# Kernel optimization log

Measured on AMD Instinct MI355X. Metric: run time of the kernel, lower is better.

Reference implementation:

```python
import jax, jax.numpy as jnp
import numpy as np

N_HEADS = 16
D_K = 64
DIM = 1024
NEG = -1e12
LN_EPS = 1e-5


def setup_inputs() -> dict:
    key = jax.random.key(0)
    ks = jax.random.split(key, 8)
    B, S, D = 2, 2048, DIM
    H, K = N_HEADS, D_K
    f = lambda k, shp: jax.random.normal(k, shp, dtype=jnp.float32)
    scale = 0.02
    return {
        "input_Q": f(ks[0], (B, S, D)),
        "input_K": f(ks[1], (B, S, D)),
        "input_V": f(ks[2], (B, S, D)),
        "attention_mask": jax.random.randint(ks[3], (B, S), 0, 2, dtype=jnp.int32),
        "W_Q": f(ks[4], (H * K, D)) * scale,  # nn.Linear weight layout [out, in]
        "W_K": f(ks[5], (H * K, D)) * scale,
        "W_V": f(ks[6], (H * K, D)) * scale,
        "W_O": f(ks[7], (D, H * K)) * scale,
        "gamma": jnp.ones((D,), jnp.float32),
        "beta": jnp.zeros((D,), jnp.float32),
    }


def reference(input_Q, input_K, input_V, attention_mask, W_Q, W_K, W_V, W_O, gamma, beta):
    B, S, D = input_Q.shape

    def proj(x, W):  # [B,S,D] @ [HK,D]^T -> [B,H,S,K]
        return (x @ W.T).reshape(B, S, N_HEADS, D_K).transpose(0, 2, 1, 3)

    Q = proj(input_Q, W_Q)
    K = proj(input_K, W_K)
    V = proj(input_V, W_V)

    scores = jnp.einsum('bhqk,bhsk->bhqs', Q, K) / np.float32(np.sqrt(D_K))

    # Faithful reproduction of scores_mask (including its inverted-looking logic):
    # mask = clamp(padding_mask + strict_upper_tri - 1, min=0); scores += (1-mask)*NEG
    am = attention_mask.astype(scores.dtype)[:, None, None, :]          # [B,1,1,S]
    low_tri = jnp.triu(jnp.ones((S, S), scores.dtype), k=1)             # 1 - tril(ones)
    m = jnp.maximum(am + low_tri - 1.0, 0.0)
    scores = scores + (1.0 - m) * NEG

    attn = jax.nn.softmax(scores, axis=-1)
    ctx = jnp.einsum('bhqs,bhsk->bhqk', attn, V)                        # [B,H,S,K]
    ctx = ctx.transpose(0, 2, 1, 3).reshape(B, S, N_HEADS * D_K)

    out = ctx @ W_O.T + input_Q                                         # fc + residual
    mu = jnp.mean(out, axis=-1, keepdims=True)
    var = jnp.var(out, axis=-1, keepdims=True)
    return (out - mu) / jnp.sqrt(var + LN_EPS) * gamma + beta
```

## Files before the change

### kernel.cpp

```cpp
#include <hip/hip_runtime.h>

#define NH    16
#define DK    64
#define DIM   1024
#define BATCH 2
#define SEQ   2048
#define MROWS (BATCH*SEQ)
#define QSCALE 0.18033688011112043f
#define SENT   -44.0f
#define PCONST 5.684341886080802e-14f

typedef unsigned short bfraw;
typedef __attribute__((ext_vector_type(8))) __bf16 bf16x8;
typedef __attribute__((ext_vector_type(4))) __bf16 bf16x4;
typedef __attribute__((ext_vector_type(8))) unsigned short u16x8;
typedef __attribute__((ext_vector_type(4))) unsigned short u16x4;
typedef __attribute__((ext_vector_type(4))) short s16x4;
typedef __attribute__((ext_vector_type(4))) float f32x4;

__device__ __forceinline__ float bf2f(bfraw u) {
    union { unsigned int i; float f; } x; x.i = ((unsigned int)u) << 16; return x.f;
}
__device__ __forceinline__ bfraw f2bf(float f) {
    union { float f; unsigned int i; } x; x.f = f;
    unsigned int r = x.i + 0x7FFFu + ((x.i >> 16) & 1u);
    return (bfraw)(r >> 16);
}
__device__ __forceinline__ bfraw f2bf_trunc(float f) {
    union { float f; unsigned int i; } x; x.f = f;
    return (bfraw)(x.i >> 16);
}
__device__ __forceinline__ float fexp2(float x) {
#if __has_builtin(__builtin_amdgcn_exp2f)
    return __builtin_amdgcn_exp2f(x);
#else
    return exp2f(x);
#endif
}

__device__ __forceinline__ f32x4 mfma16(s16x4 a, s16x4 b, f32x4 c) {
#if __has_builtin(__builtin_amdgcn_mfma_f32_16x16x16_bf16)
    union { s16x4 s; bf16x4 h; } ua, ub; ua.s = a; ub.s = b;
    return __builtin_amdgcn_mfma_f32_16x16x16_bf16(ua.h, ub.h, c, 0, 0, 0);
#elif __has_builtin(__builtin_amdgcn_mfma_f32_16x16x16bf16_1k)
    return __builtin_amdgcn_mfma_f32_16x16x16bf16_1k(a, b, c, 0, 0, 0);
#else
    asm("v_mfma_f32_16x16x16_bf16 %0, %1, %2, %0" : "+v"(c) : "v"(a), "v"(b));
    return c;
#endif
}

__device__ __forceinline__ float block_reduce(float val, float* rbuf, int op) {
    const int lane = threadIdx.x & 63, wave = threadIdx.x >> 6;
    #pragma unroll
    for (int off = 32; off; off >>= 1) {
        float o = __shfl_xor(val, off, 64);
        val = op ? (val + o) : fmaxf(val, o);
    }
    if (lane == 0) rbuf[wave] = val;
    __syncthreads();
    float r = op ? (rbuf[0] + rbuf[1] + rbuf[2] + rbuf[3])
                 : fmaxf(fmaxf(rbuf[0], rbuf[1]), fmaxf(rbuf[2], rbuf[3]));
    __syncthreads();
    return r;
}

__global__ __launch_bounds__(256) void cvt_kernel(
        const float* __restrict__ x0, const float* __restrict__ x1, const float* __restrict__ x2,
        const float* __restrict__ w0, const float* __restrict__ w1, const float* __restrict__ w2,
        const float* __restrict__ w3, bfraw* __restrict__ Xb, bfraw* __restrict__ Wb) {
    const int t = blockIdx.y;
    const float* src; bfraw* dst; int n;
    if (t < 3) { src = (t == 0) ? x0 : (t == 1) ? x1 : x2; dst = Xb + t * (MROWS * DIM); n = MROWS * DIM; }
    else { int u = t - 3; src = (u == 0) ? w0 : (u == 1) ? w1 : (u == 2) ? w2 : w3;
           dst = Wb + u * (DIM * DIM); n = DIM * DIM; }
    int idx = (blockIdx.x * 256 + threadIdx.x) * 8;
    if (idx >= n) return;
    f32x4 a = *(const f32x4*)(src + idx);
    f32x4 b = *(const f32x4*)(src + idx + 4);
    u16x8 o;
    #pragma unroll
    for (int j = 0; j < 4; j++) { o[j] = f2bf(a[j]); o[4 + j] = f2bf(b[j]); }
    *(u16x8*)(dst + idx) = o;
}

__device__ __forceinline__ void gemm128(const bfraw* __restrict__ A, const bfraw* __restrict__ B,
                                        int m0, int n0, f32x4 acc[4][4]) {
    __shared__ __align__(16) bfraw As[2][128 * 64];
    __shared__ __align__(16) bfraw Bs[2][128 * 64];
    const int tid = threadIdx.x, wave = tid >> 6;
    const int lane = tid & 63, lrow = lane & 15, quad = lane >> 4;
    const int wy = wave >> 1, wx = wave & 1;
    const int swz = lrow & 7;
    const int srow = tid >> 2;
    const int cg0  = (tid & 3) << 1;
    const int gc   = cg0 << 3;
    const int e7   = srow & 7;
    const int o0 = ((cg0 ^ e7) << 3), o1 = (((cg0 | 1) ^ e7) << 3);

    const bfraw* pa0 = A + (m0 + srow) * DIM + gc;
    const bfraw* pa1 = A + (m0 + 64 + srow) * DIM + gc;
    const bfraw* pb0 = B + (n0 + srow) * DIM + gc;
    const bfraw* pb1 = B + (n0 + 64 + srow) * DIM + gc;

    #pragma unroll
    for (int i = 0; i < 4; i++)
        #pragma unroll
        for (int j = 0; j < 4; j++) { f32x4 z = {0.f, 0.f, 0.f, 0.f}; acc[i][j] = z; }

    u16x8 ha0[4], hb0[4], ha1[4], hb1[4];

    auto LOAD = [&](u16x8 ha[4], u16x8 hb[4], int kk) {
        ha[0] = *(const u16x8*)(pa0 + kk);     ha[1] = *(const u16x8*)(pa0 + kk + 8);
        ha[2] = *(const u16x8*)(pa1 + kk);     ha[3] = *(const u16x8*)(pa1 + kk + 8);
        hb[0] = *(const u16x8*)(pb0 + kk);     hb[1] = *(const u16x8*)(pb0 + kk + 8);
        hb[2] = *(const u16x8*)(pb1 + kk);     hb[3] = *(const u16x8*)(pb1 + kk + 8);
    };
    auto STORE = [&](bfraw* Ad, bfraw* Bd, u16x8 ha[4], u16x8 hb[4]) {
        *(u16x8*)&Ad[srow * 64 + o0]        = ha[0];
        *(u16x8*)&Ad[srow * 64 + o1]        = ha[1];
        *(u16x8*)&Ad[(64 + srow) * 64 + o0] = ha[2];
        *(u16x8*)&Ad[(64 + srow) * 64 + o1] = ha[3];
        *(u16x8*)&Bd[srow * 64 + o0]        = hb[0];
        *(u16x8*)&Bd[srow * 64 + o1]        = hb[1];
        *(u16x8*)&Bd[(64 + srow) * 64 + o0] = hb[2];
        *(u16x8*)&Bd[(64 + srow) * 64 + o1] = hb[3];
    };
    auto COMPUTE = [&](const bfraw* Ad, const bfraw* Bd) {
        #pragma unroll
        for (int ks = 0; ks < 2; ks++) {
            const int c = (ks << 2) | quad;
            bf16x8 af[4], bfg[4];
            #pragma unroll
            for (int mi = 0; mi < 4; mi++)
                af[mi] = *(const bf16x8*)&Ad[(wy * 64 + mi * 16 + lrow) * 64 + ((c ^ swz) << 3)];
            #pragma unroll
            for (int ni = 0; ni < 4; ni++)
                bfg[ni] = *(const bf16x8*)&Bd[(wx * 64 + ni * 16 + lrow) * 64 + ((c ^ swz) << 3)];
            #pragma unroll
            for (int mi = 0; mi < 4; mi++)
                #pragma unroll
                for (int ni = 0; ni < 4; ni++)
                    acc[mi][ni] = __builtin_amdgcn_mfma_f32_16x16x32_bf16(af[mi], bfg[ni], acc[mi][ni], 0, 0, 0);
        }
    };

    LOAD(ha0, hb0, 0);
    LOAD(ha1, hb1, 64);

    #pragma unroll
    for (int m2 = 0; m2 < DIM / 128; m2++) {
        const int k0 = m2 * 128;
        STORE(As[0], Bs[0], ha0, hb0);
        if (k0 + 128 < DIM) LOAD(ha0, hb0, k0 + 128);
        __syncthreads();
        COMPUTE(As[0], Bs[0]);
        STORE(As[1], Bs[1], ha1, hb1);
        if (k0 + 192 < DIM) LOAD(ha1, hb1, k0 + 192);
        __syncthreads();
        COMPUTE(As[1], Bs[1]);
    }
}

__global__ __launch_bounds__(256) void qkv_gemm(
        const bfraw* __restrict__ Xb, const bfraw* __restrict__ Wb,
        bfraw* __restrict__ Qp, bfraw* __restrict__ Kp, bfraw* __restrict__ Vt) {
    const int which = blockIdx.z;
    const bfraw* A = Xb + which * (MROWS * DIM);
    const bfraw* B = Wb + which * (DIM * DIM);
    bfraw* O = (which == 0) ? Qp : (which == 1) ? Kp : Vt;
    const int m0 = blockIdx.x * 128, n0 = blockIdx.y * 128;
    f32x4 acc[4][4];
    gemm128(A, B, m0, n0, acc);
    const int lane = threadIdx.x & 63, wave = threadIdx.x >> 6;
    const int lrow = lane & 15, quad = lane >> 4;
    const int wy = wave >> 1, wx = wave & 1;
    const float scale = (which == 0) ? QSCALE : 1.0f;
    #pragma unroll
    for (int mi = 0; mi < 4; mi++)
        #pragma unroll
        for (int ni = 0; ni < 4; ni++)
            #pragma unroll
            for (int i = 0; i < 4; i++) {
                int m = m0 + wy * 64 + mi * 16 + quad * 4 + i;
                int n = n0 + wx * 64 + ni * 16 + lrow;
                int b = m >> 11, s = m & (SEQ - 1), h = n >> 6, kk = n & (DK - 1);
                bfraw v = f2bf(acc[mi][ni][i] * scale);
                if (which == 2) O[(((b * NH + h) * DK) + kk) * SEQ + s] = v;
                else            O[(((b * NH + h) * SEQ) + s) * DK + kk] = v;
            }
}

__global__ __launch_bounds__(256) void vsum_kernel(const bfraw* __restrict__ Vt,
                                                   float* __restrict__ Scum) {
    __shared__ float Ts[32][65];
    const int bh = blockIdx.x, tid = threadIdx.x;
    const int d = tid & 63, part = tid >> 6;
    const bfraw* vrow = Vt + (bh * DK + d) * SEQ;
    for (int qt = part * 8; qt < part * 8 + 8; qt++) {
        float s = 0.f;
        #pragma unroll
        for (int j = 0; j < 64; j += 8) {
            u16x8 v = *(const u16x8*)(vrow + qt * 64 + j);
            #pragma unroll
            for (int e = 0; e < 8; e++) s += bf2f(v[e]);
        }
        Ts[qt][d] = s;
    }
    __syncthreads();
    if (tid < 64) {
        float run = 0.f;
        for (int qt = 0; qt < 32; qt++) {
            Scum[(bh * 32 + qt) * 64 + tid] = run;
            run += Ts[qt][tid];
        }
    }
}

__global__ __launch_bounds__(256) void attn_flash(
        const bfraw* __restrict__ Qp, const bfraw* __restrict__ Kp, const bfraw* __restrict__ Vt,
        const float* __restrict__ Scum, const int* __restrict__ mask, bfraw* __restrict__ Ctx) {
    __shared__ __align__(16) bfraw Ks[2][64 * 64];
    __shared__ __align__(16) bfraw Vs[2][64 * 64];
    __shared__ unsigned short Mk[SEQ];
    const int bh = blockIdx.x, yy = blockIdx.y;
    const int gg = yy >> 3, jj = yy & 7;
    const int qt = (gg == 0) ? jj : (gg == 1) ? (31 - jj) : (gg == 2) ? (8 + jj) : (23 - jj);
    const int b = bh >> 4, h = bh & 15;
    const int tid = threadIdx.x, wave = tid >> 6, lane = tid & 63;
    const int lrow = lane & 15, quad = lane >> 4;
    const int baseK = ((b * NH + h) * SEQ) * DK;
    const int baseV = ((b * NH + h) * DK) * SEQ;
    const int qbase = qt * 64 + wave * 16;
    const int q_ln  = qbase + lrow;
    const int diagKt = qt * 64;
    const int ldr = tid >> 2;
    const int cg0 = (tid & 3) << 1;
    const int ldc = cg0 << 3;
    const int e7 = ldr & 7;
    const int cl0 = ((cg0 ^ e7) << 3), cl1 = (((cg0 | 1) ^ e7) << 3);

    for (int i = tid; i < SEQ; i += 256) Mk[i] = (unsigned short)(mask[b * SEQ + i] != 0);

    bf16x8 qf[2];
    qf[0] = *(const bf16x8*)(Qp + baseK + (qbase + lrow) * DK + quad * 8);
    qf[1] = *(const bf16x8*)(Qp + baseK + (qbase + lrow) * DK + 32 + quad * 8);

    f32x4 Oa[4];
    #pragma unroll
    for (int nd = 0; nd < 4; nd++) {
        f32x4 sv = *(const f32x4*)&Scum[(bh * 32 + qt) * 64 + nd * 16 + quad * 4];
        #pragma unroll
        for (int i = 0; i < 4; i++) Oa[nd][i] = PCONST * sv[i];
    }
    float lsum = 0.f;

    const int nt = (SEQ - diagKt) >> 6;
    int kt0 = diagKt;
    u16x8 k0 = *(const u16x8*)(Kp + baseK + (kt0 + ldr) * DK + ldc);
    u16x8 k1 = *(const u16x8*)(Kp + baseK + (kt0 + ldr) * DK + ldc + 8);
    u16x8 v0 = *(const u16x8*)(Vt + baseV + ldr * SEQ + kt0 + ldc);
    u16x8 v1 = *(const u16x8*)(Vt + baseV + ldr * SEQ + kt0 + ldc + 8);

    for (int t = 0; t < nt; t++, kt0 += 64) {
        bfraw* Kb = Ks[t & 1];
        bfraw* Vb = Vs[t & 1];
        *(u16x8*)&Kb[ldr * 64 + cl0] = k0;
        *(u16x8*)&Kb[ldr * 64 + cl1] = k1;
        *(u16x8*)&Vb[ldr * 64 + cl0] = v0;
        *(u16x8*)&Vb[ldr * 64 + cl1] = v1;
        if (t + 1 < nt) {
            const int kn = kt0 + 64;
            k0 = *(const u16x8*)(Kp + baseK + (kn + ldr) * DK + ldc);
            k1 = *(const u16x8*)(Kp + baseK + (kn + ldr) * DK + ldc + 8);
            v0 = *(const u16x8*)(Vt + baseV + ldr * SEQ + kn + ldc);
            v1 = *(const u16x8*)(Vt + baseV + ldr * SEQ + kn + ldc + 8);
        }
        __syncthreads();

        s16x4 pb[4];
        #pragma unroll
        for (int n = 0; n < 4; n++) {
            const int srow = n * 16 + lrow;
            bf16x8 kfa = *(const bf16x8*)&Kb[srow * 64 + ((quad ^ (lrow & 7)) << 3)];
            bf16x8 kfb = *(const bf16x8*)&Kb[srow * 64 + (((4 | quad) ^ (lrow & 7)) << 3)];
            f32x4 z = {0.f, 0.f, 0.f, 0.f};
            z = __builtin_amdgcn_mfma_f32_16x16x32_bf16(kfa, qf[0], z, 0, 0, 0);
            z = __builtin_amdgcn_mfma_f32_16x16x32_bf16(kfb, qf[1], z, 0, 0, 0);
            u16x4 pu;
            if (t == 0) {
                #pragma unroll
                for (int i = 0; i < 4; i++) {
                    int s = kt0 + n * 16 + quad * 4 + i;
                    bool valid = (Mk[s] != 0) && (s > q_ln);
                    float p = fexp2(valid ? z[i] : SENT);
                    lsum += p; pu[i] = f2bf_trunc(p);
                }
            } else {
                #pragma unroll
                for (int i = 0; i < 4; i++) {
                    int s = kt0 + n * 16 + quad * 4 + i;
                    float p = fexp2(Mk[s] ? z[i] : SENT);
                    lsum += p; pu[i] = f2bf_trunc(p);
                }
            }
            union { u16x4 u; s16x4 s; } cv; cv.u = pu; pb[n] = cv.s;
        }

        #pragma unroll
        for (int nd = 0; nd < 4; nd++) {
            const int d = nd * 16 + lrow;
            #pragma unroll
            for (int sc = 0; sc < 4; sc++) {
                s16x4 vf = *(const s16x4*)&Vb[d * 64
                    + ((((sc << 1) | (quad >> 1)) ^ (d & 7)) << 3) + ((quad & 1) << 2)];
                Oa[nd] = mfma16(vf, pb[sc], Oa[nd]);
            }
        }
    }

    float r = lsum;
    r += __shfl_xor(r, 16, 64);
    r += __shfl_xor(r, 32, 64);
    const float inv = 1.0f / (r + (float)diagKt * PCONST);
    #pragma unroll
    for (int nd = 0; nd < 4; nd++) {
        u16x4 o;
        #pragma unroll
        for (int i = 0; i < 4; i++) o[i] = f2bf(Oa[nd][i] * inv);
        *(u16x4*)&Ctx[(b * SEQ + q_ln) * DIM + h * DK + nd * 16 + quad * 4] = o;
    }
}

__global__ __launch_bounds__(256) void out_gemm(
        const bfraw* __restrict__ Ctx, const bfraw* __restrict__ WoB, float* __restrict__ C) {
    const int m0 = blockIdx.x * 128, n0 = blockIdx.y * 128;
    f32x4 acc[4][4];
    gemm128(Ctx, WoB, m0, n0, acc);
    const int lane = threadIdx.x & 63, wave = threadIdx.x >> 6;
    const int lrow = lane & 15, quad = lane >> 4;
    const int wy = wave >> 1, wx = wave & 1;
    #pragma unroll
    for (int mi = 0; mi < 4; mi++)
        #pragma unroll
        for (int ni = 0; ni < 4; ni++)
            #pragma unroll
            for (int i = 0; i < 4; i++) {
                int m = m0 + wy * 64 + mi * 16 + quad * 4 + i;
                int n = n0 + wx * 64 + ni * 16 + lrow;
                C[m * DIM + n] = acc[mi][ni][i];
            }
}

__global__ __launch_bounds__(256) void ln_kernel(
        const float* __restrict__ C, const float* __restrict__ Xq,
        const float* __restrict__ gamma, const float* __restrict__ beta,
        float* __restrict__ out) {
    __shared__ float rbuf[4];
    const int m = blockIdx.x, tid = threadIdx.x;
    const float* crow = C + m * DIM;
    const float* xrow = Xq + m * DIM;
    float v[4]; float s = 0.f, s2 = 0.f;
    #pragma unroll
    for (int i = 0; i < 4; i++) {
        int d = tid + (i << 8);
        float x = crow[d] + xrow[d];
        v[i] = x; s += x; s2 += x * x;
    }
    float S  = block_reduce(s,  rbuf, 1);
    float S2 = block_reduce(s2, rbuf, 1);
    float mu  = S * (1.0f / DIM);
    float var = S2 * (1.0f / DIM) - mu * mu;
    float rstd = rsqrtf(var + 1e-5f);
    #pragma unroll
    for (int i = 0; i < 4; i++) {
        int d = tid + (i << 8);
        out[m * DIM + d] = (v[i] - mu) * rstd * gamma[d] + beta[d];
    }
}

extern "C" void kernel_launch(void* const* d_in, const int* in_sizes, int n_in,
                              void* d_out, int out_size, void* d_ws, size_t ws_size,
                              hipStream_t stream) {
    const float* Xq    = (const float*)d_in[0];
    const float* Xk    = (const float*)d_in[1];
    const float* Xv    = (const float*)d_in[2];
    const int*   mask  = (const int*)  d_in[3];
    const float* Wq    = (const float*)d_in[4];
    const float* Wk    = (const float*)d_in[5];
    const float* Wv    = (const float*)d_in[6];
    const float* Wo    = (const float*)d_in[7];
    const float* gamma = (const float*)d_in[8];
    const float* beta  = (const float*)d_in[9];
    float* out = (float*)d_out;

    char* ws = (char*)d_ws;
    bfraw* Xb   = (bfraw*)(ws);
    bfraw* Wb   = (bfraw*)(ws + (24u << 20));
    bfraw* Qp   = (bfraw*)(ws + (32u << 20));
    bfraw* Kp   = (bfraw*)(ws + (40u << 20));
    bfraw* Vt   = (bfraw*)(ws + (48u << 20));
    bfraw* Ctx  = (bfraw*)(ws + (56u << 20));
    float* C    = (float*)(ws);
    float* Scum = (float*)(ws + (16u << 20));

    dim3 blk(256);
    cvt_kernel<<<dim3(MROWS * DIM / (256 * 8), 7), blk, 0, stream>>>(Xq, Xk, Xv, Wq, Wk, Wv, Wo, Xb, Wb);
    qkv_gemm  <<<dim3(MROWS / 128, DIM / 128, 3),  blk, 0, stream>>>(Xb, Wb, Qp, Kp, Vt);
    vsum_kernel<<<dim3(BATCH * NH),                blk, 0, stream>>>(Vt, Scum);
    attn_flash<<<dim3(BATCH * NH, SEQ / 64),       blk, 0, stream>>>(Qp, Kp, Vt, Scum, mask, Ctx);
    out_gemm  <<<dim3(MROWS / 128, DIM / 128),     blk, 0, stream>>>(Ctx, Wb + 3 * (DIM * DIM), C);
    ln_kernel <<<dim3(MROWS),                      blk, 0, stream>>>(C, Xq, gamma, beta, out);
}
```

Measured before the change: 224.0 us.

## Process two query sub-tiles per attention block to reuse K/V tiles

Each attention workgroup now handles a 128-row query tile, with every wave owning two 16-row query groups 64 rows apart. Each K/V tile loaded into shared memory therefore feeds twice as many MFMAs, which halves the grid and the global K/V traffic. The diagonal masking now spans the first two key tiles, and the block-to-tile order is simplified. In exchange there are fewer blocks (512) and more registers per thread, and the coarser tiles worsen load balance in the triangular workload.

Result: faster. 219.5 us (-2.0%).

```diff
diff --git a/kernel.cpp b/kernel.cpp
--- a/kernel.cpp
+++ b/kernel.cpp
@@ -217,6 +217,38 @@
     }
 }
 
+template<bool NEAR>
+__device__ __forceinline__ void qk_soft(
+        const bfraw* Kb, const bf16x8 qa[2], const bf16x8 qb[2],
+        const unsigned short* Mk, int kt0, int lrow, int quad, int q0, int q1,
+        float& ls0, float& ls1, s16x4 p0[4], s16x4 p1[4]) {
+    #pragma unroll
+    for (int n = 0; n < 4; n++) {
+        const int srow = n * 16 + lrow;
+        bf16x8 kfa = *(const bf16x8*)&Kb[srow * 64 + ((quad ^ (lrow & 7)) << 3)];
+        bf16x8 kfb = *(const bf16x8*)&Kb[srow * 64 + (((4 | quad) ^ (lrow & 7)) << 3)];
+        f32x4 z0 = {0.f, 0.f, 0.f, 0.f}, z1 = {0.f, 0.f, 0.f, 0.f};
+        z0 = __builtin_amdgcn_mfma_f32_16x16x32_bf16(kfa, qa[0], z0, 0, 0, 0);
+        z0 = __builtin_amdgcn_mfma_f32_16x16x32_bf16(kfb, qa[1], z0, 0, 0, 0);
+        z1 = __builtin_amdgcn_mfma_f32_16x16x32_bf16(kfa, qb[0], z1, 0, 0, 0);
+        z1 = __builtin_amdgcn_mfma_f32_16x16x32_bf16(kfb, qb[1], z1, 0, 0, 0);
+        u16x4 u0, u1;
+        #pragma unroll
+        for (int i = 0; i < 4; i++) {
+            int s = kt0 + n * 16 + quad * 4 + i;
+            bool m = (Mk[s] != 0);
+            bool va = NEAR ? (m && s > q0) : m;
+            bool vb = NEAR ? (m && s > q1) : m;
+            float pa = fexp2(va ? z0[i] : SENT);
+            float pb = fexp2(vb ? z1[i] : SENT);
+            ls0 += pa; ls1 += pb;
+            u0[i] = f2bf_trunc(pa); u1[i] = f2bf_trunc(pb);
+        }
+        union { u16x4 u; s16x4 s; } c0, c1; c0.u = u0; c1.u = u1;
+        p0[n] = c0.s; p1[n] = c1.s;
+    }
+}
+
 __global__ __launch_bounds__(256) void attn_flash(
         const bfraw* __restrict__ Qp, const bfraw* __restrict__ Kp, const bfraw* __restrict__ Vt,
         const float* __restrict__ Scum, const int* __restrict__ mask, bfraw* __restrict__ Ctx) {
@@ -225,15 +257,16 @@
     __shared__ unsigned short Mk[SEQ];
     const int bh = blockIdx.x, yy = blockIdx.y;
     const int gg = yy >> 3, jj = yy & 7;
-    const int qt = (gg == 0) ? jj : (gg == 1) ? (31 - jj) : (gg == 2) ? (8 + jj) : (23 - jj);
+    const int qt = gg ? (15 - jj) : jj;
     const int b = bh >> 4, h = bh & 15;
     const int tid = threadIdx.x, wave = tid >> 6, lane = tid & 63;
     const int lrow = lane & 15, quad = lane >> 4;
     const int baseK = ((b * NH + h) * SEQ) * DK;
     const int baseV = ((b * NH + h) * DK) * SEQ;
-    const int qbase = qt * 64 + wave * 16;
-    const int q_ln  = qbase + lrow;
-    const int diagKt = qt * 64;
+    const int qbase = qt * 128 + wave * 16;
+    const int q0 = qbase + lrow;
+    const int q1 = q0 + 64;
+    const int diagKt = qt * 128;
     const int ldr = tid >> 2;
     const int cg0 = (tid & 3) << 1;
     const int ldc = cg0 << 3;
@@ -242,18 +275,21 @@
 
     for (int i = tid; i < SEQ; i += 256) Mk[i] = (unsigned short)(mask[b * SEQ + i] != 0);
 
-    bf16x8 qf[2];
-    qf[0] = *(const bf16x8*)(Qp + baseK + (qbase + lrow) * DK + quad * 8);
-    qf[1] = *(const bf16x8*)(Qp + baseK + (qbase + lrow) * DK + 32 + quad * 8);
-
-    f32x4 Oa[4];
+    bf16x8 qa[2], qb[2];
+    qa[0] = *(const bf16x8*)(Qp + baseK + q0 * DK + quad * 8);
+    qa[1] = *(const bf16x8*)(Qp + baseK + q0 * DK + 32 + quad * 8);
+    qb[0] = *(const bf16x8*)(Qp + baseK + q1 * DK + quad * 8);
+    qb[1] = *(const bf16x8*)(Qp + baseK + q1 * DK + 32 + quad * 8);
+
+    f32x4 Oa[4], Ob[4];
+    const int scb = (bh * 32 + 2 * qt) * 64;
     #pragma unroll
     for (int nd = 0; nd < 4; nd++) {
-        f32x4 sv = *(const f32x4*)&Scum[(bh * 32 + qt) * 64 + nd * 16 + quad * 4];
-        #pragma unroll
-        for (int i = 0; i < 4; i++) Oa[nd][i] = PCONST * sv[i];
-    }
-    float lsum = 0.f;
+        f32x4 sv = *(const f32x4*)&Scum[scb + nd * 16 + quad * 4];
+        #pragma unroll
+        for (int i = 0; i < 4; i++) { Oa[nd][i] = PCONST * sv[i]; Ob[nd][i] = PCONST * sv[i]; }
+    }
+    float ls0 = 0.f, ls1 = 0.f;
 
     const int nt = (SEQ - diagKt) >> 6;
     int kt0 = diagKt;
@@ -278,34 +314,9 @@
         }
         __syncthreads();
 
-        s16x4 pb[4];
-        #pragma unroll
-        for (int n = 0; n < 4; n++) {
-            const int srow = n * 16 + lrow;
-            bf16x8 kfa = *(const bf16x8*)&Kb[srow * 64 + ((quad ^ (lrow & 7)) << 3)];
-            bf16x8 kfb = *(const bf16x8*)&Kb[srow * 64 + (((4 | quad) ^ (lrow & 7)) << 3)];
-            f32x4 z = {0.f, 0.f, 0.f, 0.f};
-            z = __builtin_amdgcn_mfma_f32_16x16x32_bf16(kfa, qf[0], z, 0, 0, 0);
-            z = __builtin_amdgcn_mfma_f32_16x16x32_bf16(kfb, qf[1], z, 0, 0, 0);
-            u16x4 pu;
-            if (t == 0) {
-                #pragma unroll
-                for (int i = 0; i < 4; i++) {
-                    int s = kt0 + n * 16 + quad * 4 + i;
-                    bool valid = (Mk[s] != 0) && (s > q_ln);
-                    float p = fexp2(valid ? z[i] : SENT);
-                    lsum += p; pu[i] = f2bf_trunc(p);
-                }
-            } else {
-                #pragma unroll
-                for (int i = 0; i < 4; i++) {
-                    int s = kt0 + n * 16 + quad * 4 + i;
-                    float p = fexp2(Mk[s] ? z[i] : SENT);
-                    lsum += p; pu[i] = f2bf_trunc(p);
-                }
-            }
-            union { u16x4 u; s16x4 s; } cv; cv.u = pu; pb[n] = cv.s;
-        }
+        s16x4 p0[4], p1[4];
+        if (t < 2) qk_soft<true >(Kb, qa, qb, Mk, kt0, lrow, quad, q0, q1, ls0, ls1, p0, p1);
+        else       qk_soft<false>(Kb, qa, qb, Mk, kt0, lrow, quad, q0, q1, ls0, ls1, p0, p1);
 
         #pragma unroll
         for (int nd = 0; nd < 4; nd++) {
@@ -314,21 +325,30 @@
             for (int sc = 0; sc < 4; sc++) {
                 s16x4 vf = *(const s16x4*)&Vb[d * 64
                     + ((((sc << 1) | (quad >> 1)) ^ (d & 7)) << 3) + ((quad & 1) << 2)];
-                Oa[nd] = mfma16(vf, pb[sc], Oa[nd]);
+                Oa[nd] = mfma16(vf, p0[sc], Oa[nd]);
+                Ob[nd] = mfma16(vf, p1[sc], Ob[nd]);
             }
         }
     }
 
-    float r = lsum;
-    r += __shfl_xor(r, 16, 64);
-    r += __shfl_xor(r, 32, 64);
-    const float inv = 1.0f / (r + (float)diagKt * PCONST);
+    float r0 = ls0;
+    r0 += __shfl_xor(r0, 16, 64);
+    r0 += __shfl_xor(r0, 32, 64);
+    float r1 = ls1;
+    r1 += __shfl_xor(r1, 16, 64);
+    r1 += __shfl_xor(r1, 32, 64);
+    const float inv0 = 1.0f / (r0 + (float)diagKt * PCONST);
+    const float inv1 = 1.0f / (r1 + (float)diagKt * PCONST);
     #pragma unroll
     for (int nd = 0; nd < 4; nd++) {
-        u16x4 o;
-        #pragma unroll
-        for (int i = 0; i < 4; i++) o[i] = f2bf(Oa[nd][i] * inv);
-        *(u16x4*)&Ctx[(b * SEQ + q_ln) * DIM + h * DK + nd * 16 + quad * 4] = o;
+        u16x4 oA, oB;
+        #pragma unroll
+        for (int i = 0; i < 4; i++) {
+            oA[i] = f2bf(Oa[nd][i] * inv0);
+            oB[i] = f2bf(Ob[nd][i] * inv1);
+        }
+        *(u16x4*)&Ctx[(b * SEQ + q0) * DIM + h * DK + nd * 16 + quad * 4] = oA;
+        *(u16x4*)&Ctx[(b * SEQ + q1) * DIM + h * DK + nd * 16 + quad * 4] = oB;
     }
 }
 
@@ -408,7 +428,7 @@
     cvt_kernel<<<dim3(MROWS * DIM / (256 * 8), 7), blk, 0, stream>>>(Xq, Xk, Xv, Wq, Wk, Wv, Wo, Xb, Wb);
     qkv_gemm  <<<dim3(MROWS / 128, DIM / 128, 3),  blk, 0, stream>>>(Xb, Wb, Qp, Kp, Vt);
     vsum_kernel<<<dim3(BATCH * NH),                blk, 0, stream>>>(Vt, Scum);
-    attn_flash<<<dim3(BATCH * NH, SEQ / 64),       blk, 0, stream>>>(Qp, Kp, Vt, Scum, mask, Ctx);
+    attn_flash<<<dim3(BATCH * NH, SEQ / 128),      blk, 0, stream>>>(Qp, Kp, Vt, Scum, mask, Ctx);
     out_gemm  <<<dim3(MROWS / 128, DIM / 128),     blk, 0, stream>>>(Ctx, Wb + 3 * (DIM * DIM), C);
     ln_kernel <<<dim3(MROWS),                      blk, 0, stream>>>(C, Xq, gamma, beta, out);
 }
```

## Widen attention query tile to 128 rows with 512-thread blocks

Applied to the files above, without the earlier changes.

The flash attention kernel now processes 128 query rows per block with 8 waves, so each K/V tile staged in shared memory is reused by twice as many queries and each thread loads half as much per tile. The mask is stored as floats and applied with an FMA blend instead of a select, and the probability conversion uses the native bf16 cast (round-to-nearest) instead of truncation. The causal-diagonal handling now covers the first two KV tiles, and the block-order remap is adjusted for 16 query tiles. The trade-off is fewer blocks, coarser load balancing across the triangular workload, and higher per-block resource use.

Result: faster. 219.2 us (-2.1%).

```diff
diff --git a/kernel.cpp b/kernel.cpp
--- a/kernel.cpp
+++ b/kernel.cpp
@@ -25,10 +25,6 @@
     union { float f; unsigned int i; } x; x.f = f;
     unsigned int r = x.i + 0x7FFFu + ((x.i >> 16) & 1u);
     return (bfraw)(r >> 16);
-}
-__device__ __forceinline__ bfraw f2bf_trunc(float f) {
-    union { float f; unsigned int i; } x; x.f = f;
-    return (bfraw)(x.i >> 16);
 }
 __device__ __forceinline__ float fexp2(float x) {
 #if __has_builtin(__builtin_amdgcn_exp2f)
@@ -217,39 +213,65 @@
     }
 }
 
-__global__ __launch_bounds__(256) void attn_flash(
+template<bool NEAR>
+__device__ __forceinline__ void qk_soft(
+        const bfraw* Kb, const bf16x8 qf[2], const float* Mkf,
+        int kt0, int lrow, int quad, int q_ln, float& lsum, s16x4 pb[4]) {
+    #pragma unroll
+    for (int n = 0; n < 4; n++) {
+        const int srow = n * 16 + lrow;
+        bf16x8 kfa = *(const bf16x8*)&Kb[srow * 64 + ((quad ^ (lrow & 7)) << 3)];
+        bf16x8 kfb = *(const bf16x8*)&Kb[srow * 64 + (((4 | quad) ^ (lrow & 7)) << 3)];
+        f32x4 z = {0.f, 0.f, 0.f, 0.f};
+        z = __builtin_amdgcn_mfma_f32_16x16x32_bf16(kfa, qf[0], z, 0, 0, 0);
+        z = __builtin_amdgcn_mfma_f32_16x16x32_bf16(kfb, qf[1], z, 0, 0, 0);
+        f32x4 mv = *(const f32x4*)&Mkf[kt0 + n * 16 + quad * 4];
+        union { bf16x4 h; s16x4 s; } pk;
+        #pragma unroll
+        for (int i = 0; i < 4; i++) {
+            float m = mv[i];
+            if (NEAR) { int s = kt0 + n * 16 + quad * 4 + i; m = (s > q_ln) ? m : 0.0f; }
+            float p = fexp2(fmaf(m, z[i] - SENT, SENT));
+            lsum += p;
+            pk.h[i] = (__bf16)p;
+        }
+        pb[n] = pk.s;
+    }
+}
+
+__global__ __launch_bounds__(512) void attn_flash(
         const bfraw* __restrict__ Qp, const bfraw* __restrict__ Kp, const bfraw* __restrict__ Vt,
         const float* __restrict__ Scum, const int* __restrict__ mask, bfraw* __restrict__ Ctx) {
     __shared__ __align__(16) bfraw Ks[2][64 * 64];
     __shared__ __align__(16) bfraw Vs[2][64 * 64];
-    __shared__ unsigned short Mk[SEQ];
+    __shared__ float Mkf[SEQ];
     const int bh = blockIdx.x, yy = blockIdx.y;
     const int gg = yy >> 3, jj = yy & 7;
-    const int qt = (gg == 0) ? jj : (gg == 1) ? (31 - jj) : (gg == 2) ? (8 + jj) : (23 - jj);
+    const int qt = gg ? (15 - jj) : jj;
     const int b = bh >> 4, h = bh & 15;
     const int tid = threadIdx.x, wave = tid >> 6, lane = tid & 63;
     const int lrow = lane & 15, quad = lane >> 4;
     const int baseK = ((b * NH + h) * SEQ) * DK;
     const int baseV = ((b * NH + h) * DK) * SEQ;
-    const int qbase = qt * 64 + wave * 16;
+    const int qbase = qt * 128 + wave * 16;
     const int q_ln  = qbase + lrow;
-    const int diagKt = qt * 64;
-    const int ldr = tid >> 2;
-    const int cg0 = (tid & 3) << 1;
-    const int ldc = cg0 << 3;
-    const int e7 = ldr & 7;
-    const int cl0 = ((cg0 ^ e7) << 3), cl1 = (((cg0 | 1) ^ e7) << 3);
-
-    for (int i = tid; i < SEQ; i += 256) Mk[i] = (unsigned short)(mask[b * SEQ + i] != 0);
+    const int diagKt = qt * 128;
+    const int ldr = tid >> 3;
+    const int c8  = tid & 7;
+    const int ldc = c8 << 3;
+    const int cl  = ((c8 ^ (ldr & 7)) << 3);
+
+    for (int i = tid; i < SEQ; i += 512) Mkf[i] = (mask[b * SEQ + i] != 0) ? 1.0f : 0.0f;
 
     bf16x8 qf[2];
-    qf[0] = *(const bf16x8*)(Qp + baseK + (qbase + lrow) * DK + quad * 8);
-    qf[1] = *(const bf16x8*)(Qp + baseK + (qbase + lrow) * DK + 32 + quad * 8);
+    qf[0] = *(const bf16x8*)(Qp + baseK + q_ln * DK + quad * 8);
+    qf[1] = *(const bf16x8*)(Qp + baseK + q_ln * DK + 32 + quad * 8);
 
     f32x4 Oa[4];
+    const int scb = (bh * 32 + 2 * qt) * 64;
     #pragma unroll
     for (int nd = 0; nd < 4; nd++) {
-        f32x4 sv = *(const f32x4*)&Scum[(bh * 32 + qt) * 64 + nd * 16 + quad * 4];
+        f32x4 sv = *(const f32x4*)&Scum[scb + nd * 16 + quad * 4];
         #pragma unroll
         for (int i = 0; i < 4; i++) Oa[nd][i] = PCONST * sv[i];
     }
@@ -258,54 +280,23 @@
     const int nt = (SEQ - diagKt) >> 6;
     int kt0 = diagKt;
     u16x8 k0 = *(const u16x8*)(Kp + baseK + (kt0 + ldr) * DK + ldc);
-    u16x8 k1 = *(const u16x8*)(Kp + baseK + (kt0 + ldr) * DK + ldc + 8);
     u16x8 v0 = *(const u16x8*)(Vt + baseV + ldr * SEQ + kt0 + ldc);
-    u16x8 v1 = *(const u16x8*)(Vt + baseV + ldr * SEQ + kt0 + ldc + 8);
 
     for (int t = 0; t < nt; t++, kt0 += 64) {
         bfraw* Kb = Ks[t & 1];
         bfraw* Vb = Vs[t & 1];
-        *(u16x8*)&Kb[ldr * 64 + cl0] = k0;
-        *(u16x8*)&Kb[ldr * 64 + cl1] = k1;
-        *(u16x8*)&Vb[ldr * 64 + cl0] = v0;
-        *(u16x8*)&Vb[ldr * 64 + cl1] = v1;
+        *(u16x8*)&Kb[ldr * 64 + cl] = k0;
+        *(u16x8*)&Vb[ldr * 64 + cl] = v0;
         if (t + 1 < nt) {
             const int kn = kt0 + 64;
             k0 = *(const u16x8*)(Kp + baseK + (kn + ldr) * DK + ldc);
-            k1 = *(const u16x8*)(Kp + baseK + (kn + ldr) * DK + ldc + 8);
             v0 = *(const u16x8*)(Vt + baseV + ldr * SEQ + kn + ldc);
-            v1 = *(const u16x8*)(Vt + baseV + ldr * SEQ + kn + ldc + 8);
         }
         __syncthreads();
 
         s16x4 pb[4];
-        #pragma unroll
-        for (int n = 0; n < 4; n++) {
-            const int srow = n * 16 + lrow;
-            bf16x8 kfa = *(const bf16x8*)&Kb[srow * 64 + ((quad ^ (lrow & 7)) << 3)];
-            bf16x8 kfb = *(const bf16x8*)&Kb[srow * 64 + (((4 | quad) ^ (lrow & 7)) << 3)];
-            f32x4 z = {0.f, 0.f, 0.f, 0.f};
-            z = __builtin_amdgcn_mfma_f32_16x16x32_bf16(kfa, qf[0], z, 0, 0, 0);
-            z = __builtin_amdgcn_mfma_f32_16x16x32_bf16(kfb, qf[1], z, 0, 0, 0);
-            u16x4 pu;
-            if (t == 0) {
-                #pragma unroll
-                for (int i = 0; i < 4; i++) {
-                    int s = kt0 + n * 16 + quad * 4 + i;
-                    bool valid = (Mk[s] != 0) && (s > q_ln);
-                    float p = fexp2(valid ? z[i] : SENT);
-                    lsum += p; pu[i] = f2bf_trunc(p);
-                }
-            } else {
-                #pragma unroll
-                for (int i = 0; i < 4; i++) {
-                    int s = kt0 + n * 16 + quad * 4 + i;
-                    float p = fexp2(Mk[s] ? z[i] : SENT);
-                    lsum += p; pu[i] = f2bf_trunc(p);
-                }
-            }
-            union { u16x4 u; s16x4 s; } cv; cv.u = pu; pb[n] = cv.s;
-        }
+        if (t < 2) qk_soft<true >(Kb, qf, Mkf, kt0, lrow, quad, q_ln, lsum, pb);
+        else       qk_soft<false>(Kb, qf, Mkf, kt0, lrow, quad, q_ln, lsum, pb);
 
         #pragma unroll
         for (int nd = 0; nd < 4; nd++) {
@@ -408,7 +399,7 @@
     cvt_kernel<<<dim3(MROWS * DIM / (256 * 8), 7), blk, 0, stream>>>(Xq, Xk, Xv, Wq, Wk, Wv, Wo, Xb, Wb);
     qkv_gemm  <<<dim3(MROWS / 128, DIM / 128, 3),  blk, 0, stream>>>(Xb, Wb, Qp, Kp, Vt);
     vsum_kernel<<<dim3(BATCH * NH),                blk, 0, stream>>>(Vt, Scum);
-    attn_flash<<<dim3(BATCH * NH, SEQ / 64),       blk, 0, stream>>>(Qp, Kp, Vt, Scum, mask, Ctx);
+    attn_flash<<<dim3(BATCH * NH, SEQ / 128),      dim3(512), 0, stream>>>(Qp, Kp, Vt, Scum, mask, Ctx);
     out_gemm  <<<dim3(MROWS / 128, DIM / 128),     blk, 0, stream>>>(Ctx, Wb + 3 * (DIM * DIM), C);
     ln_kernel <<<dim3(MROWS),                      blk, 0, stream>>>(C, Xq, gamma, beta, out);
 }
```
